# Optimization experiments

Hardware: AMD Instinct MI355X
Metric: run time of the kernel (lower is better)

Reference implementation:

```python
import jax, jax.numpy as jnp
import numpy as np

B, S, H, I, E, K = 8, 4096, 512, 2048, 8, 2

def setup_inputs() -> dict:
    key = jax.random.key(0)
    ks = jax.random.split(key, 7)
    sH = 1.0 / np.sqrt(H)
    sI = 1.0 / np.sqrt(I)
    return {
        "x": jax.random.normal(ks[0], (B, S, H), dtype=jnp.float32),
        "gate_w": jax.random.uniform(ks[1], (H, E), jnp.float32, -sH, sH),
        "gate_b": jnp.zeros((E,), jnp.float32),
        "w1": jax.random.uniform(ks[2], (E, H, I), jnp.float32, -sH, sH),
        "b1": jax.random.uniform(ks[3], (E, I), jnp.float32, -sH, sH),
        "w2": jax.random.uniform(ks[4], (E, I, H), jnp.float32, -sI, sI),
        "b2": jax.random.uniform(ks[5], (E, H), jnp.float32, -sI, sI),
    }

def reference(x, gate_w, gate_b, w1, b1, w2, b2):
    # Gating: softmax over experts, top-k, renormalize selected probs via softmax.
    gate_probs = jax.nn.softmax(x @ gate_w + gate_b, axis=-1)          # [B,S,E]
    top_v, top_i = jax.lax.top_k(gate_probs, K)                        # [B,S,K]
    top_w = jax.nn.softmax(top_v, axis=-1)                             # renormalized
    out = jnp.zeros_like(x)
    for e in range(E):  # small fixed expert count
        # combine weight per token for expert e (0 if not routed here)
        ce = jnp.sum(jnp.where(top_i == e, top_w, 0.0), axis=-1)       # [B,S]
        h = jax.nn.relu(jnp.einsum("bsh,hi->bsi", x, w1[e]) + b1[e])   # [B,S,I]
        ye = jnp.einsum("bsi,ih->bsh", h, w2[e]) + b2[e]               # [B,S,H]
        out = out + ce[..., None] * ye
    return out
```

## Files before the change

### kernel.cpp

```cpp
#include <hip/hip_runtime.h>
#include <hip/hip_bf16.h>
#include <cstdint>

#define T_TOK 32768
#define HD 512
#define ID 2048
#define NE 8

typedef __bf16 bf16x8 __attribute__((ext_vector_type(8)));
typedef float f32x4 __attribute__((ext_vector_type(4)));

__device__ __forceinline__ ushort f2bf(float f) {
  __hip_bfloat16 h = __float2bfloat16(f);
  return *reinterpret_cast<ushort*>(&h);
}

__device__ __forceinline__ void gload16(const ushort* g, ushort* l) {
  __builtin_amdgcn_global_load_lds((__attribute__((address_space(1))) void*)(void*)g,
                                   (__attribute__((address_space(3))) void*)(void*)l,
                                   16, 0, 0);
}

__global__ void k_zero(float4* out4, int n4, int* counts) {
  if (blockIdx.x == 0 && threadIdx.x < NE) counts[threadIdx.x] = 0;
  float4 z = make_float4(0.f, 0.f, 0.f, 0.f);
  for (int i = blockIdx.x * blockDim.x + threadIdx.x; i < n4; i += gridDim.x * blockDim.x)
    out4[i] = z;
}

__global__ void k_transpose(const float* __restrict__ in, ushort* __restrict__ out, int R, int C) {
  __shared__ float tile[32][33];
  int z = blockIdx.z;
  const float* src = in + (size_t)z * R * C;
  ushort* dst = out + (size_t)z * R * C;
  int c0 = blockIdx.x * 32, r0 = blockIdx.y * 32;
  int tx = threadIdx.x, ty = threadIdx.y;
#pragma unroll
  for (int i = 0; i < 32; i += 8)
    tile[ty + i][tx] = src[(size_t)(r0 + ty + i) * C + c0 + tx];
  __syncthreads();
#pragma unroll
  for (int i = 0; i < 32; i += 8)
    dst[(size_t)(c0 + ty + i) * R + r0 + tx] = f2bf(tile[tx][ty + i]);
}

__global__ __launch_bounds__(256) void k_cast_gate(const float* __restrict__ x,
                                                   const float* __restrict__ gw,
                                                   const float* __restrict__ gb,
                                                   ushort* __restrict__ xb,
                                                   uchar2* __restrict__ tope,
                                                   float2* __restrict__ tw) {
  int t = blockIdx.x * 4 + (threadIdx.x >> 6);
  int lane = threadIdx.x & 63;
  const float4* xr = (const float4*)(x + (size_t)t * HD);
  float4 v0 = xr[lane];
  float4 v1 = xr[lane + 64];
  ushort4 o0, o1;
  o0.x = f2bf(v0.x); o0.y = f2bf(v0.y); o0.z = f2bf(v0.z); o0.w = f2bf(v0.w);
  o1.x = f2bf(v1.x); o1.y = f2bf(v1.y); o1.z = f2bf(v1.z); o1.w = f2bf(v1.w);
  ushort4* xw = (ushort4*)(xb + (size_t)t * HD);
  xw[lane] = o0;
  xw[lane + 64] = o1;
  float xv[8] = {v0.x, v0.y, v0.z, v0.w, v1.x, v1.y, v1.z, v1.w};
  float p[8] = {0, 0, 0, 0, 0, 0, 0, 0};
  const float* g0 = gw + (size_t)lane * 4 * 8;
  const float* g1 = gw + (size_t)(256 + lane * 4) * 8;
#pragma unroll
  for (int j = 0; j < 4; ++j)
#pragma unroll
    for (int e = 0; e < 8; ++e) p[e] += xv[j] * g0[j * 8 + e];
#pragma unroll
  for (int j = 0; j < 4; ++j)
#pragma unroll
    for (int e = 0; e < 8; ++e) p[e] += xv[4 + j] * g1[j * 8 + e];
#pragma unroll
  for (int e = 0; e < 8; ++e) {
    float s = p[e];
    for (int off = 32; off; off >>= 1) s += __shfl_xor(s, off);
    p[e] = s + gb[e];
  }
  float mx = p[0];
#pragma unroll
  for (int e = 1; e < 8; ++e) mx = fmaxf(mx, p[e]);
  float Z = 0.f;
  float pr[8];
#pragma unroll
  for (int e = 0; e < 8; ++e) { pr[e] = expf(p[e] - mx); Z += pr[e]; }
  float invZ = 1.f / Z;
#pragma unroll
  for (int e = 0; e < 8; ++e) pr[e] *= invZ;
  float v1v = pr[0]; int i1 = 0;
#pragma unroll
  for (int e = 1; e < 8; ++e) { if (pr[e] > v1v) { v1v = pr[e]; i1 = e; } }
  float v2v = -1.f; int i2 = 0;
#pragma unroll
  for (int e = 0; e < 8; ++e) { if (e != i1 && pr[e] > v2v) { v2v = pr[e]; i2 = e; } }
  float c1 = 1.f / (1.f + expf(v2v - v1v));
  float c2 = 1.f - c1;
  if (lane == 0) {
    tope[t] = make_uchar2((unsigned char)i1, (unsigned char)i2);
    tw[t] = make_float2(c1, c2);
  }
}

__global__ __launch_bounds__(256) void k_route(const uchar2* __restrict__ tope,
                                               const float2* __restrict__ tw,
                                               int* __restrict__ rtok, float* __restrict__ rw,
                                               int* __restrict__ counts) {
  int t = blockIdx.x * 256 + threadIdx.x;
  int lane = threadIdx.x & 63;
  uchar2 ei = tope[t];
  float2 c = tw[t];
  unsigned long long below = (1ull << lane) - 1ull;
#pragma unroll
  for (int e = 0; e < NE; ++e) {
    bool sel = (ei.x == e) || (ei.y == e);
    unsigned long long mask = __ballot(sel);
    if (mask == 0ull) continue;
    int cnt = __popcll(mask);
    int base = 0;
    if (lane == 0) base = atomicAdd(&counts[e], cnt);
    base = __shfl(base, 0);
    if (sel) {
      int pos = base + __popcll(mask & below);
      rtok[e * T_TOK + pos] = t;
      rw[e * T_TOK + pos] = (ei.x == e) ? c.x : c.y;
    }
  }
}

__global__ __launch_bounds__(256) void k_ffn1(const ushort* __restrict__ xb,
                                              const ushort* __restrict__ w1t,
                                              const float* __restrict__ b1,
                                              const int* __restrict__ rtok,
                                              const int* __restrict__ counts,
                                              ushort* __restrict__ h, int e, int cbase) {
  int cnt = counts[e];
  int m0 = cbase + blockIdx.x * 128;
  if (m0 >= cnt) return;
  int n0 = blockIdx.y * 128;
  __shared__ __attribute__((aligned(16))) ushort As[128 * 32];
  __shared__ __attribute__((aligned(16))) ushort Bs[128 * 32];
  int tid = threadIdx.x, lane = tid & 63, wv = tid >> 6;
  int c0id = wv * 128 + lane, c1id = c0id + 64;
  int rA0 = c0id >> 2, rA1 = c1id >> 2;
  int kq0 = (c0id & 3) * 8, kq1 = (c1id & 3) * 8;
  const int* rte = rtok + e * T_TOK;
  int tok0 = rte[min(m0 + rA0, cnt - 1)];
  int tok1 = rte[min(m0 + rA1, cnt - 1)];
  const ushort* aSrc0 = xb + (size_t)tok0 * HD + kq0;
  const ushort* aSrc1 = xb + (size_t)tok1 * HD + kq1;
  const ushort* bBase = w1t + ((size_t)e * ID + n0) * HD;
  const ushort* bSrc0 = bBase + (size_t)rA0 * HD + kq0;
  const ushort* bSrc1 = bBase + (size_t)rA1 * HD + kq1;
  ushort* aDst = As + (size_t)wv * 128 * 8;
  ushort* bDst = Bs + (size_t)wv * 128 * 8;
  f32x4 acc[4][4] = {};
  int lr = lane & 15, lk = lane >> 4;
  int wr = wv >> 1, wc = wv & 1;
  const ushort* aRd = As + ((wr * 64 + lr) * 32 + lk * 8);
  const ushort* bRd = Bs + ((wc * 64 + lr) * 32 + lk * 8);
  for (int k0 = 0; k0 < HD; k0 += 32) {
    gload16(aSrc0 + k0, aDst);
    gload16(aSrc1 + k0, aDst + 64 * 8);
    gload16(bSrc0 + k0, bDst);
    gload16(bSrc1 + k0, bDst + 64 * 8);
    __syncthreads();
    bf16x8 af[4], bfr[4];
#pragma unroll
    for (int i = 0; i < 4; ++i) {
      af[i] = *(const bf16x8*)(aRd + i * 16 * 32);
      bfr[i] = *(const bf16x8*)(bRd + i * 16 * 32);
    }
#pragma unroll
    for (int mi = 0; mi < 4; ++mi)
#pragma unroll
      for (int ni = 0; ni < 4; ++ni)
        acc[mi][ni] = __builtin_amdgcn_mfma_f32_16x16x32_bf16(af[mi], bfr[ni], acc[mi][ni], 0, 0, 0);
    __syncthreads();
  }
  int hrow0 = blockIdx.x * 128;
#pragma unroll
  for (int ni = 0; ni < 4; ++ni) {
    int ng = n0 + wc * 64 + ni * 16 + lr;
    float bv = b1[e * ID + ng];
#pragma unroll
    for (int mi = 0; mi < 4; ++mi) {
      int rbase = hrow0 + wr * 64 + mi * 16 + lk * 4;
#pragma unroll
      for (int r = 0; r < 4; ++r) {
        float v = acc[mi][ni][r] + bv;
        v = fmaxf(v, 0.f);
        h[(size_t)(rbase + r) * ID + ng] = f2bf(v);
      }
    }
  }
}

__global__ __launch_bounds__(256) void k_ffn2(const ushort* __restrict__ h,
                                              const ushort* __restrict__ w2t,
                                              const float* __restrict__ b2,
                                              const int* __restrict__ rtok,
                                              const float* __restrict__ rw,
                                              const int* __restrict__ counts,
                                              float* __restrict__ out, int e, int cbase) {
  int cnt = counts[e];
  int m0 = cbase + blockIdx.x * 128;
  if (m0 >= cnt) return;
  int n0 = blockIdx.y * 128;
  __shared__ __attribute__((aligned(16))) ushort As[128 * 32];
  __shared__ __attribute__((aligned(16))) ushort Bs[128 * 32];
  __shared__ int stok[128];
  __shared__ float scoef[128];
  int tid = threadIdx.x, lane = tid & 63, wv = tid >> 6;
  if (tid < 128) {
    int idx = min(m0 + tid, cnt - 1);
    stok[tid] = rtok[e * T_TOK + idx];
    scoef[tid] = rw[e * T_TOK + idx];
  }
  int c0id = wv * 128 + lane, c1id = c0id + 64;
  int rA0 = c0id >> 2, rA1 = c1id >> 2;
  int kq0 = (c0id & 3) * 8, kq1 = (c1id & 3) * 8;
  int hrow0 = blockIdx.x * 128;
  const ushort* aSrc0 = h + (size_t)(hrow0 + rA0) * ID + kq0;
  const ushort* aSrc1 = h + (size_t)(hrow0 + rA1) * ID + kq1;
  const ushort* bBase = w2t + ((size_t)e * HD + n0) * ID;
  const ushort* bSrc0 = bBase + (size_t)rA0 * ID + kq0;
  const ushort* bSrc1 = bBase + (size_t)rA1 * ID + kq1;
  ushort* aDst = As + (size_t)wv * 128 * 8;
  ushort* bDst = Bs + (size_t)wv * 128 * 8;
  f32x4 acc[4][4] = {};
  int lr = lane & 15, lk = lane >> 4;
  int wr = wv >> 1, wc = wv & 1;
  const ushort* aRd = As + ((wr * 64 + lr) * 32 + lk * 8);
  const ushort* bRd = Bs + ((wc * 64 + lr) * 32 + lk * 8);
  for (int k0 = 0; k0 < ID; k0 += 32) {
    gload16(aSrc0 + k0, aDst);
    gload16(aSrc1 + k0, aDst + 64 * 8);
    gload16(bSrc0 + k0, bDst);
    gload16(bSrc1 + k0, bDst + 64 * 8);
    __syncthreads();
    bf16x8 af[4], bfr[4];
#pragma unroll
    for (int i = 0; i < 4; ++i) {
      af[i] = *(const bf16x8*)(aRd + i * 16 * 32);
      bfr[i] = *(const bf16x8*)(bRd + i * 16 * 32);
    }
#pragma unroll
    for (int mi = 0; mi < 4; ++mi)
#pragma unroll
      for (int ni = 0; ni < 4; ++ni)
        acc[mi][ni] = __builtin_amdgcn_mfma_f32_16x16x32_bf16(af[mi], bfr[ni], acc[mi][ni], 0, 0, 0);
    __syncthreads();
  }
#pragma unroll
  for (int ni = 0; ni < 4; ++ni) {
    int ng = n0 + wc * 64 + ni * 16 + lr;
    float b2v = b2[e * HD + ng];
#pragma unroll
    for (int mi = 0; mi < 4; ++mi) {
      int rloc = wr * 64 + mi * 16 + lk * 4;
#pragma unroll
      for (int r = 0; r < 4; ++r) {
        int m_l = rloc + r;
        if (m0 + m_l < cnt) {
          float v = (acc[mi][ni][r] + b2v) * scoef[m_l];
          size_t oi = (size_t)stok[m_l] * HD + ng;
          out[oi] += v;
        }
      }
    }
  }
}

extern "C" void kernel_launch(void* const* d_in, const int* in_sizes, int n_in,
                              void* d_out, int out_size, void* d_ws, size_t ws_size,
                              hipStream_t stream) {
  const float* x  = (const float*)d_in[0];
  const float* gw = (const float*)d_in[1];
  const float* gb = (const float*)d_in[2];
  const float* w1 = (const float*)d_in[3];
  const float* b1 = (const float*)d_in[4];
  const float* w2 = (const float*)d_in[5];
  const float* b2 = (const float*)d_in[6];
  float* out = (float*)d_out;

  char* p = (char*)d_ws;
  ushort* xb   = (ushort*)p; p += (size_t)T_TOK * HD * 2;
  ushort* w1t  = (ushort*)p; p += (size_t)NE * ID * HD * 2;
  ushort* w2t  = (ushort*)p; p += (size_t)NE * HD * ID * 2;
  int*    rtok = (int*)p;    p += (size_t)NE * T_TOK * 4;
  float*  rw   = (float*)p;  p += (size_t)NE * T_TOK * 4;
  uchar2* tope = (uchar2*)p; p += (size_t)T_TOK * 2;
  float2* tw   = (float2*)p; p += (size_t)T_TOK * 8;
  int*  counts = (int*)p;    p += 128;
  ushort* hbuf = (ushort*)p;
  size_t fixed = (size_t)(p - (char*)d_ws);
  size_t avail = ws_size > fixed ? ws_size - fixed : 0;

  int MC;
  if ((size_t)32768 * ID * 2 <= avail)      MC = 32768;
  else if ((size_t)16384 * ID * 2 <= avail) MC = 16384;
  else if ((size_t)8192 * ID * 2 <= avail)  MC = 8192;
  else                                      MC = 4096;
  int nchunk = (T_TOK + MC - 1) / MC;

  k_zero<<<2048, 256, 0, stream>>>((float4*)out, T_TOK * HD / 4, counts);
  k_cast_gate<<<T_TOK / 4, 256, 0, stream>>>(x, gw, gb, xb, tope, tw);
  k_route<<<T_TOK / 256, 256, 0, stream>>>(tope, tw, rtok, rw, counts);
  k_transpose<<<dim3(ID / 32, HD / 32, NE), dim3(32, 8), 0, stream>>>(w1, w1t, HD, ID);
  k_transpose<<<dim3(HD / 32, ID / 32, NE), dim3(32, 8), 0, stream>>>(w2, w2t, ID, HD);

  for (int e = 0; e < NE; ++e) {
    for (int c = 0; c < nchunk; ++c) {
      k_ffn1<<<dim3(MC / 128, ID / 128), 256, 0, stream>>>(xb, w1t, b1, rtok, counts, hbuf, e, c * MC);
      k_ffn2<<<dim3(MC / 128, HD / 128), 256, 0, stream>>>(hbuf, w2t, b2, rtok, rw, counts, out, e, c * MC);
    }
  }
}
```

Before: 1.120 ms.

## Batch all experts into one launch per chunk via blockIdx.z

Instead of looping over experts on the host with separate FFN1/FFN2 launches, all experts are processed concurrently using a third grid dimension, with a per-expert hidden buffer slice. Since different experts now write overlapping output rows concurrently, the output accumulation switches to atomic float adds. This removes many serialized launches and the tail underutilization of small per-expert grids, at the cost of more workspace, atomic traffic and possibly smaller chunks if workspace is limited.

```diff
diff --git a/kernel.cpp b/kernel.cpp
--- a/kernel.cpp
+++ b/kernel.cpp
@@ -134,7 +134,8 @@
                                               const float* __restrict__ b1,
                                               const int* __restrict__ rtok,
                                               const int* __restrict__ counts,
-                                              ushort* __restrict__ h, int e, int cbase) {
+                                              ushort* __restrict__ h, int cbase, int MC) {
+  int e = blockIdx.z;
   int cnt = counts[e];
   int m0 = cbase + blockIdx.x * 128;
   if (m0 >= cnt) return;
@@ -179,6 +180,7 @@
         acc[mi][ni] = __builtin_amdgcn_mfma_f32_16x16x32_bf16(af[mi], bfr[ni], acc[mi][ni], 0, 0, 0);
     __syncthreads();
   }
+  ushort* he = h + (size_t)e * MC * ID;
   int hrow0 = blockIdx.x * 128;
 #pragma unroll
   for (int ni = 0; ni < 4; ++ni) {
@@ -191,7 +193,7 @@
       for (int r = 0; r < 4; ++r) {
         float v = acc[mi][ni][r] + bv;
         v = fmaxf(v, 0.f);
-        h[(size_t)(rbase + r) * ID + ng] = f2bf(v);
+        he[(size_t)(rbase + r) * ID + ng] = f2bf(v);
       }
     }
   }
@@ -203,7 +205,8 @@
                                               const int* __restrict__ rtok,
                                               const float* __restrict__ rw,
                                               const int* __restrict__ counts,
-                                              float* __restrict__ out, int e, int cbase) {
+                                              float* __restrict__ out, int cbase, int MC) {
+  int e = blockIdx.z;
   int cnt = counts[e];
   int m0 = cbase + blockIdx.x * 128;
   if (m0 >= cnt) return;
@@ -222,8 +225,9 @@
   int rA0 = c0id >> 2, rA1 = c1id >> 2;
   int kq0 = (c0id & 3) * 8, kq1 = (c1id & 3) * 8;
   int hrow0 = blockIdx.x * 128;
-  const ushort* aSrc0 = h + (size_t)(hrow0 + rA0) * ID + kq0;
-  const ushort* aSrc1 = h + (size_t)(hrow0 + rA1) * ID + kq1;
+  const ushort* he = h + (size_t)e * MC * ID;
+  const ushort* aSrc0 = he + (size_t)(hrow0 + rA0) * ID + kq0;
+  const ushort* aSrc1 = he + (size_t)(hrow0 + rA1) * ID + kq1;
   const ushort* bBase = w2t + ((size_t)e * HD + n0) * ID;
   const ushort* bSrc0 = bBase + (size_t)rA0 * ID + kq0;
   const ushort* bSrc1 = bBase + (size_t)rA1 * ID + kq1;
@@ -265,8 +269,7 @@
         int m_l = rloc + r;
         if (m0 + m_l < cnt) {
           float v = (acc[mi][ni][r] + b2v) * scoef[m_l];
-          size_t oi = (size_t)stok[m_l] * HD + ng;
-          out[oi] += v;
+          unsafeAtomicAdd(&out[(size_t)stok[m_l] * HD + ng], v);
         }
       }
     }
@@ -298,12 +301,12 @@
   size_t fixed = (size_t)(p - (char*)d_ws);
   size_t avail = ws_size > fixed ? ws_size - fixed : 0;
 
-  int MC;
-  if ((size_t)32768 * ID * 2 <= avail)      MC = 32768;
-  else if ((size_t)16384 * ID * 2 <= avail) MC = 16384;
-  else if ((size_t)8192 * ID * 2 <= avail)  MC = 8192;
-  else                                      MC = 4096;
+  int MC = 256;
+  for (int cand = 8192; cand >= 256; cand >>= 1) {
+    if ((size_t)NE * cand * ID * 2 <= avail) { MC = cand; break; }
+  }
   int nchunk = (T_TOK + MC - 1) / MC;
+  int MCB = MC / 128 > 0 ? MC / 128 : 1;
 
   k_zero<<<2048, 256, 0, stream>>>((float4*)out, T_TOK * HD / 4, counts);
   k_cast_gate<<<T_TOK / 4, 256, 0, stream>>>(x, gw, gb, xb, tope, tw);
@@ -311,10 +314,10 @@
   k_transpose<<<dim3(ID / 32, HD / 32, NE), dim3(32, 8), 0, stream>>>(w1, w1t, HD, ID);
   k_transpose<<<dim3(HD / 32, ID / 32, NE), dim3(32, 8), 0, stream>>>(w2, w2t, ID, HD);
 
-  for (int e = 0; e < NE; ++e) {
-    for (int c = 0; c < nchunk; ++c) {
-      k_ffn1<<<dim3(MC / 128, ID / 128), 256, 0, stream>>>(xb, w1t, b1, rtok, counts, hbuf, e, c * MC);
-      k_ffn2<<<dim3(MC / 128, HD / 128), 256, 0, stream>>>(hbuf, w2t, b2, rtok, rw, counts, out, e, c * MC);
-    }
-  }
-}
+  for (int c = 0; c < nchunk; ++c) {
+    k_ffn1<<<dim3(MCB, ID / 128, NE), 256, 0, stream>>>(xb, w1t, b1, rtok, counts,
+                                                        hbuf, c * MC, MC);
+    k_ffn2<<<dim3(MCB, HD / 128, NE), 256, 0, stream>>>(hbuf, w2t, b2, rtok, rw, counts,
+                                                        out, c * MC, MC);
+  }
+}
```

Result: faster. 947.9 us (-15.3%).

## Batch all experts into padded grouped windows and split-K the second FFN GEMM

Applied to the files above, without the earlier changes.

Replaces the per-expert launch loop with grouped GEMM launches over a concatenated, 128-row-padded expert row space. Each block finds its expert from device-computed prefix offsets, which cuts the number of kernel launches and the idle blocks that early-exit on small experts. The second GEMM is split into two K halves along a third grid dimension and accumulates into the output with atomic adds, giving more blocks on the narrow N=512 output. The cost is atomic traffic on the output and nondeterministic float summation order.

```diff
diff --git a/kernel.cpp b/kernel.cpp
--- a/kernel.cpp
+++ b/kernel.cpp
@@ -6,6 +6,7 @@
 #define HD 512
 #define ID 2048
 #define NE 8
+#define ROWS_PAD_MAX 66560
 
 typedef __bf16 bf16x8 __attribute__((ext_vector_type(8)));
 typedef float f32x4 __attribute__((ext_vector_type(4)));
@@ -129,15 +130,38 @@
   }
 }
 
+__global__ void k_offsets(const int* __restrict__ counts, int* __restrict__ poff) {
+  if (threadIdx.x == 0) {
+    int acc = 0;
+    poff[0] = 0;
+#pragma unroll
+    for (int e = 0; e < NE; ++e) {
+      acc += ((counts[e] + 127) >> 7) << 7;
+      poff[e + 1] = acc;
+    }
+  }
+}
+
+__device__ __forceinline__ int find_expert(const int* poff, int v) {
+  int e = 0;
+#pragma unroll
+  for (int j = 1; j < NE; ++j) e += (v >= poff[j]) ? 1 : 0;
+  return e;
+}
+
 __global__ __launch_bounds__(256) void k_ffn1(const ushort* __restrict__ xb,
                                               const ushort* __restrict__ w1t,
                                               const float* __restrict__ b1,
                                               const int* __restrict__ rtok,
                                               const int* __restrict__ counts,
-                                              ushort* __restrict__ h, int e, int cbase) {
+                                              const int* __restrict__ poff,
+                                              ushort* __restrict__ h, int wb128) {
+  int mb = wb128 + blockIdx.x;
+  int v = mb << 7;
+  if (v >= poff[NE]) return;
+  int e = find_expert(poff, v);
   int cnt = counts[e];
-  int m0 = cbase + blockIdx.x * 128;
-  if (m0 >= cnt) return;
+  int m0 = v - poff[e];
   int n0 = blockIdx.y * 128;
   __shared__ __attribute__((aligned(16))) ushort As[128 * 32];
   __shared__ __attribute__((aligned(16))) ushort Bs[128 * 32];
@@ -189,9 +213,9 @@
       int rbase = hrow0 + wr * 64 + mi * 16 + lk * 4;
 #pragma unroll
       for (int r = 0; r < 4; ++r) {
-        float v = acc[mi][ni][r] + bv;
-        v = fmaxf(v, 0.f);
-        h[(size_t)(rbase + r) * ID + ng] = f2bf(v);
+        float v2 = acc[mi][ni][r] + bv;
+        v2 = fmaxf(v2, 0.f);
+        h[(size_t)(rbase + r) * ID + ng] = f2bf(v2);
       }
     }
   }
@@ -203,11 +227,16 @@
                                               const int* __restrict__ rtok,
                                               const float* __restrict__ rw,
                                               const int* __restrict__ counts,
-                                              float* __restrict__ out, int e, int cbase) {
+                                              const int* __restrict__ poff,
+                                              float* __restrict__ out, int wb128) {
+  int mb = wb128 + blockIdx.x;
+  int v = mb << 7;
+  if (v >= poff[NE]) return;
+  int e = find_expert(poff, v);
   int cnt = counts[e];
-  int m0 = cbase + blockIdx.x * 128;
-  if (m0 >= cnt) return;
+  int m0 = v - poff[e];
   int n0 = blockIdx.y * 128;
+  int ks = blockIdx.z;
   __shared__ __attribute__((aligned(16))) ushort As[128 * 32];
   __shared__ __attribute__((aligned(16))) ushort Bs[128 * 32];
   __shared__ int stok[128];
@@ -234,7 +263,8 @@
   int wr = wv >> 1, wc = wv & 1;
   const ushort* aRd = As + ((wr * 64 + lr) * 32 + lk * 8);
   const ushort* bRd = Bs + ((wc * 64 + lr) * 32 + lk * 8);
-  for (int k0 = 0; k0 < ID; k0 += 32) {
+  int kbeg = ks * (ID / 2), kend = kbeg + ID / 2;
+  for (int k0 = kbeg; k0 < kend; k0 += 32) {
     gload16(aSrc0 + k0, aDst);
     gload16(aSrc1 + k0, aDst + 64 * 8);
     gload16(bSrc0 + k0, bDst);
@@ -256,7 +286,7 @@
 #pragma unroll
   for (int ni = 0; ni < 4; ++ni) {
     int ng = n0 + wc * 64 + ni * 16 + lr;
-    float b2v = b2[e * HD + ng];
+    float b2v = (ks == 0) ? b2[e * HD + ng] : 0.f;
 #pragma unroll
     for (int mi = 0; mi < 4; ++mi) {
       int rloc = wr * 64 + mi * 16 + lk * 4;
@@ -264,9 +294,8 @@
       for (int r = 0; r < 4; ++r) {
         int m_l = rloc + r;
         if (m0 + m_l < cnt) {
-          float v = (acc[mi][ni][r] + b2v) * scoef[m_l];
-          size_t oi = (size_t)stok[m_l] * HD + ng;
-          out[oi] += v;
+          float vv = (acc[mi][ni][r] + b2v) * scoef[m_l];
+          unsafeAtomicAdd(&out[(size_t)stok[m_l] * HD + ng], vv);
         }
       }
     }
@@ -293,28 +322,31 @@
   float*  rw   = (float*)p;  p += (size_t)NE * T_TOK * 4;
   uchar2* tope = (uchar2*)p; p += (size_t)T_TOK * 2;
   float2* tw   = (float2*)p; p += (size_t)T_TOK * 8;
-  int*  counts = (int*)p;    p += 128;
+  int*  counts = (int*)p;
+  int*  poff   = counts + 16;
+  p += 128;
   ushort* hbuf = (ushort*)p;
   size_t fixed = (size_t)(p - (char*)d_ws);
   size_t avail = ws_size > fixed ? ws_size - fixed : 0;
 
-  int MC;
-  if ((size_t)32768 * ID * 2 <= avail)      MC = 32768;
-  else if ((size_t)16384 * ID * 2 <= avail) MC = 16384;
-  else if ((size_t)8192 * ID * 2 <= avail)  MC = 8192;
-  else                                      MC = 4096;
-  int nchunk = (T_TOK + MC - 1) / MC;
+  int Wmax = (int)((avail / ((size_t)ID * 2)) & ~(size_t)127);
+  if (Wmax > ROWS_PAD_MAX) Wmax = ROWS_PAD_MAX;
+  int W = (Wmax >= 16640) ? 16640 : Wmax;
+  if (W < 128) W = 128;
+  int nwin = (ROWS_PAD_MAX + W - 1) / W;
+  int WB = W / 128;
 
   k_zero<<<2048, 256, 0, stream>>>((float4*)out, T_TOK * HD / 4, counts);
   k_cast_gate<<<T_TOK / 4, 256, 0, stream>>>(x, gw, gb, xb, tope, tw);
   k_route<<<T_TOK / 256, 256, 0, stream>>>(tope, tw, rtok, rw, counts);
+  k_offsets<<<1, 64, 0, stream>>>(counts, poff);
   k_transpose<<<dim3(ID / 32, HD / 32, NE), dim3(32, 8), 0, stream>>>(w1, w1t, HD, ID);
   k_transpose<<<dim3(HD / 32, ID / 32, NE), dim3(32, 8), 0, stream>>>(w2, w2t, ID, HD);
 
-  for (int e = 0; e < NE; ++e) {
-    for (int c = 0; c < nchunk; ++c) {
-      k_ffn1<<<dim3(MC / 128, ID / 128), 256, 0, stream>>>(xb, w1t, b1, rtok, counts, hbuf, e, c * MC);
-      k_ffn2<<<dim3(MC / 128, HD / 128), 256, 0, stream>>>(hbuf, w2t, b2, rtok, rw, counts, out, e, c * MC);
-    }
-  }
-}
+  for (int w = 0; w < nwin; ++w) {
+    int wb128 = w * WB;
+    k_ffn1<<<dim3(WB, ID / 128), 256, 0, stream>>>(xb, w1t, b1, rtok, counts, poff, hbuf, wb128);
+    k_ffn2<<<dim3(WB, HD / 128, 2), 256, 0, stream>>>(hbuf, w2t, b2, rtok, rw, counts, poff,
+                                                      out, wb128);
+  }
+}
```

Result: faster. 1.043 ms (-6.8%).
